# Performance work log

Measured on AMD Instinct MI355X. Metric: run time of the kernel, lower is better.

## Reference

```python
import jax, jax.numpy as jnp
import numpy as np

NEG_SLOPE = 0.2

def gat_conv(x, src, dst, W, a_src, a_dst, b, num_nodes, concat):
    # PyG GATConv (add_self_loops already applied to src/dst).
    H, C = a_src.shape
    h = (x @ W).reshape(-1, H, C)                      # [N,H,C]
    s = jnp.einsum('nhc,hc->nh', h, a_src)             # per-node src score
    d = jnp.einsum('nhc,hc->nh', h, a_dst)             # per-node dst score
    e = jax.nn.leaky_relu(s[src] + d[dst], NEG_SLOPE)  # [E,H]
    emax = jax.lax.stop_gradient(
        jax.ops.segment_max(e, dst, num_segments=num_nodes))  # [N,H]
    ex = jnp.exp(e - emax[dst])
    denom = jax.ops.segment_sum(ex, dst, num_segments=num_nodes)
    alpha = ex / denom[dst]                            # segment softmax over in-edges
    msg = h[src] * alpha[:, :, None]                   # [E,H,C]
    out = jax.ops.segment_sum(msg, dst, num_segments=num_nodes)
    out = out.reshape(num_nodes, H * C) if concat else out.mean(axis=1)
    return out + b

def setup_inputs() -> dict:
    key = jax.random.key(0)
    ks = jax.random.split(key, 20)
    N, E, F = 50000, 400000, 256
    x = jax.random.normal(ks[0], (N, F), dtype=jnp.float32)
    edge_index = jax.random.randint(ks[1], (2, E), 0, N, dtype=jnp.int64)
    def p(k, shape):
        return (jax.random.normal(k, shape, dtype=jnp.float32) * 0.1)
    inp = {'x': x, 'edge_index': edge_index}
    # conv1: 256 -> 8x32 ; conv2: 256 -> 4x32 ; conv3: 128 -> 2x32 ; conv4: 64 -> 1x32
    dims = [(256, 8, 32), (256, 4, 32), (128, 2, 32), (64, 1, 32)]
    ki = 2
    for i, (fin, H, C) in enumerate(dims, start=1):
        inp[f'W{i}'] = p(ks[ki], (fin, H * C)); ki += 1
        inp[f'a_src{i}'] = p(ks[ki], (H, C)); ki += 1
        inp[f'a_dst{i}'] = p(ks[ki], (H, C)); ki += 1
        bdim = H * C if i < 4 else C
        inp[f'b{i}'] = jnp.zeros((bdim,), dtype=jnp.float32)
    return inp

def reference(x, edge_index, W1, a_src1, a_dst1, b1, W2, a_src2, a_dst2, b2,
              W3, a_src3, a_dst3, b3, W4, a_src4, a_dst4, b4):
    N = x.shape[0]
    loops = jnp.arange(N, dtype=edge_index.dtype)
    src = jnp.concatenate([edge_index[0], loops])
    dst = jnp.concatenate([edge_index[1], loops])
    h = jax.nn.elu(gat_conv(x, src, dst, W1, a_src1, a_dst1, b1, N, True))
    h = jax.nn.elu(gat_conv(h, src, dst, W2, a_src2, a_dst2, b2, N, True))
    h = gat_conv(h, src, dst, W3, a_src3, a_dst3, b3, N, True)
    h = jax.nn.elu(h)
    h = gat_conv(h, src, dst, W4, a_src4, a_dst4, b4, N, False)
    return jax.nn.log_softmax(h, axis=1)
```

## Files before the change

### kernel.cpp

```cpp
#include <hip/hip_runtime.h>
#include <hip/hip_bf16.h>

#define LRELU_SLOPE 0.2f

typedef __attribute__((ext_vector_type(8))) short short8;
typedef __attribute__((ext_vector_type(4))) float f32x4;

__device__ __forceinline__ unsigned short bf16r(float f) {
    unsigned int u = __builtin_bit_cast(unsigned int, f);
    u += 0x7fffu + ((u >> 16) & 1u);
    return (unsigned short)(u >> 16);
}
__device__ __forceinline__ float bf2f(unsigned short u) {
    return __builtin_bit_cast(float, (unsigned int)u << 16);
}

#define GLD16(g, l)                                                            \
    __builtin_amdgcn_global_load_lds(                                          \
        (const __attribute__((address_space(1))) void*)(g),                    \
        (__attribute__((address_space(3))) void*)(l), 16, 0, 0)


#define WTOT 108544

__global__ void k_pre(const float* __restrict__ x, unsigned short* __restrict__ Xb,
                      const float* __restrict__ Wa, const float* __restrict__ Wb,
                      const float* __restrict__ Wc, const float* __restrict__ Wd,
                      unsigned short* __restrict__ Ta, unsigned short* __restrict__ Tb,
                      unsigned short* __restrict__ Tc, unsigned short* __restrict__ Td,
                      const int* __restrict__ ei, int* __restrict__ cnt,
                      int XC, int E, int N) {
    int gid = blockIdx.x * blockDim.x + threadIdx.x;
    if (gid < XC) {
        const float4* xp = (const float4*)x + (long)gid * 2;
        float4 a = xp[0], b = xp[1];
        short8 pk;
        pk[0] = (short)bf16r(a.x); pk[1] = (short)bf16r(a.y);
        pk[2] = (short)bf16r(a.z); pk[3] = (short)bf16r(a.w);
        pk[4] = (short)bf16r(b.x); pk[5] = (short)bf16r(b.y);
        pk[6] = (short)bf16r(b.z); pk[7] = (short)bf16r(b.w);
        *(short8*)(Xb + (long)gid * 8) = pk;
        return;
    }
    int id = gid - XC;
    if (id < WTOT) {
        const float* W; unsigned short* T; int K, Nc;
        if (id < 65536)       { W = Wa; T = Ta; K = 256; Nc = 256; }
        else if (id < 98304)  { id -= 65536;  W = Wb; T = Tb; K = 256; Nc = 128; }
        else if (id < 106496) { id -= 98304;  W = Wc; T = Tc; K = 128; Nc = 64; }
        else                  { id -= 106496; W = Wd; T = Td; K = 64;  Nc = 32; }
        int n = id / K, k = id % K;
        T[id] = bf16r(W[(long)k * Nc + n]);
        return;
    }
    int e = id - WTOT;
    if (e >= E + N) return;
    int dst = (e < E) ? ei[E + e] : (e - E);
    atomicAdd(&cnt[dst], 1);
}


__global__ void k_scan_blk(const int* __restrict__ cnt, int* __restrict__ offs,
                           int* __restrict__ bsum, int N) {
    __shared__ int temp[1024];
    int t = threadIdx.x;
    int gi = blockIdx.x * 1024 + t;
    int v = (gi < N) ? cnt[gi] : 0;
    temp[t] = v;
    __syncthreads();
    for (int o = 1; o < 1024; o <<= 1) {
        int x = (t >= o) ? temp[t - o] : 0;
        __syncthreads();
        temp[t] += x;
        __syncthreads();
    }
    if (gi < N) offs[gi] = temp[t] - v;
    if (t == 1023) bsum[blockIdx.x] = temp[1023];
}

__global__ void k_scan(const int* __restrict__ cnt, int* __restrict__ offs, int N) {
    __shared__ int temp[1024];
    __shared__ int carry_s;
    int t = threadIdx.x;
    if (t == 0) carry_s = 0;
    __syncthreads();
    for (int base = 0; base < N; base += 1024) {
        int v = (base + t < N) ? cnt[base + t] : 0;
        temp[t] = v;
        __syncthreads();
        for (int o = 1; o < 1024; o <<= 1) {
            int x = (t >= o) ? temp[t - o] : 0;
            __syncthreads();
            temp[t] += x;
            __syncthreads();
        }
        int incl = temp[t];
        int carry = carry_s;
        if (base + t < N) offs[base + t] = carry + incl - v;
        __syncthreads();
        if (t == 1023) carry_s = carry + temp[1023];
        __syncthreads();
    }
    if (t == 0) offs[N] = carry_s;
}

__global__ void k_scan_add(int* __restrict__ offs, const int* __restrict__ bpre,
                           int* __restrict__ wp, int N, int nb) {
    int gi = blockIdx.x * blockDim.x + threadIdx.x;
    if (gi < N) {
        int v = offs[gi] + bpre[gi >> 10];
        offs[gi] = v;
        wp[gi] = v;
    } else if (gi == N) {
        offs[N] = bpre[nb];
    }
}

__global__ void k_scatter(const int* __restrict__ ei, int* __restrict__ wp,
                          int* __restrict__ adj, int E, int N) {
    int e = blockIdx.x * blockDim.x + threadIdx.x;
    if (e >= E + N) return;
    int srcn = (e < E) ? ei[e] : (e - E);
    int dst  = (e < E) ? ei[E + e] : (e - E);
    int pos = atomicAdd(&wp[dst], 1);
    adj[pos] = srcn;
}


template<int BN, int KT, int GX>
__global__ __launch_bounds__(256) void k_mgemm(const unsigned short* __restrict__ Ab,
                                               const unsigned short* __restrict__ WT,
                                               unsigned short* __restrict__ Cb,
                                               const float* __restrict__ a_src,
                                               const float* __restrict__ a_dst,
                                               float* __restrict__ sbuf,
                                               float* __restrict__ dbuf,
                                               int M, int Nc, int H, int RB) {
    constexpr int KITER = KT / 32;
    constexpr int NBF = BN / 16;
    constexpr int CPR = BN / 32;
    constexpr int SP  = BN + 8;
    constexpr int ASH = 64 * KT;
    constexpr int BSH = BN * KT;
    constexpr int EPIL = 64 * SP;
    constexpr int LBSZ = (ASH + BSH) > EPIL ? (ASH + BSH) : EPIL;
    constexpr int SHC = (KT == 256) ? 5 : (KT == 128 ? 4 : 3);
    constexpr int BIT = BN * KT / 2048;
    __shared__ __align__(16) unsigned short LB[LBSZ];

    int id = blockIdx.x;
    int xcd = id & 7;
    int q  = id >> 3;
    int ct = q % GX;
    int rb = (q / GX) * 8 + xcd;
    if (rb >= RB) return;
    int bm = rb * 64, bn = ct * BN;

    int t = threadIdx.x;
    int wv = t >> 6, l = t & 63;
    int row_in = l & 15, quad = l >> 4;
    char* LBb = (char*)LB;

    long abyte = (long)bm * (KT * 2);
    long mbyte = (long)M * (KT * 2);
    const char* Agb = (const char*)Ab;
#pragma unroll
    for (int i = 0; i < KITER; ++i) {
        int c = i * 256 + t;
        int cs = c ^ ((c >> SHC) & 7);
        long gb = abyte + (long)cs * 16;
        if (gb >= mbyte) gb = abyte;
        GLD16(Agb + gb, LBb + (i * 256 + wv * 64) * 16);
    }
    const char* WTb = (const char*)WT + (long)bn * (KT * 2);
#pragma unroll
    for (int i = 0; i < BIT; ++i) {
        int c = i * 256 + t;
        int cs = c ^ ((c >> SHC) & 7);
        GLD16(WTb + (long)cs * 16, LBb + ASH * 2 + (i * 256 + wv * 64) * 16);
    }
    asm volatile("s_waitcnt vmcnt(0)" ::: "memory");
    __syncthreads();

    f32x4 acc[NBF];
#pragma unroll
    for (int j = 0; j < NBF; ++j) acc[j] = (f32x4){0.f, 0.f, 0.f, 0.f};

    int arow = wv * 16 + row_in;
#pragma unroll
    for (int ki = 0; ki < KITER; ++ki) {
        int aoff = (arow * (KT * 2) + ki * 64 + quad * 16) ^ ((arow & 7) << 4);
        short8 av = *(const short8*)(LBb + aoff);
#pragma unroll
        for (int f = 0; f < NBF; ++f) {
            int bcol = f * 16 + row_in;
            int boff = ASH * 2 + ((bcol * (KT * 2) + ki * 64 + quad * 16) ^ ((bcol & 7) << 4));
            short8 bv = *(const short8*)(LBb + boff);
            acc[f] = __builtin_amdgcn_mfma_f32_16x16x32_bf16(av, bv, acc[f], 0, 0, 0);
        }
    }
    __syncthreads();

#pragma unroll
    for (int r = 0; r < 4; ++r)
#pragma unroll
        for (int f = 0; f < NBF; ++f)
            LB[(wv * 16 + quad * 4 + r) * SP + f * 16 + row_in] = bf16r(acc[f][r]);
    __syncthreads();

    int rr = t / CPR, cc = t % CPR;
    if (rr < 64) {
        int grow = bm + rr;
        int colb = bn + cc * 32;
        if (grow < M && colb < Nc) {
            const unsigned short* ep = &LB[rr * SP + cc * 32];
            short8 v0 = *(const short8*)(ep);
            short8 v1 = *(const short8*)(ep + 8);
            short8 v2 = *(const short8*)(ep + 16);
            short8 v3 = *(const short8*)(ep + 24);
            unsigned short* cp = &Cb[(long)grow * Nc + colb];
            *(short8*)(cp)      = v0;
            *(short8*)(cp + 8)  = v1;
            *(short8*)(cp + 16) = v2;
            *(short8*)(cp + 24) = v3;
            int hd = colb >> 5;
            const float* ap = a_src + hd * 32;
            const float* dp = a_dst + hd * 32;
            float ss = 0.f, dd = 0.f;
#pragma unroll
            for (int u = 0; u < 8; ++u) {
                float va = bf2f((unsigned short)v0[u]); ss += va * ap[u];      dd += va * dp[u];
                float vb = bf2f((unsigned short)v1[u]); ss += vb * ap[8 + u];  dd += vb * dp[8 + u];
                float vc = bf2f((unsigned short)v2[u]); ss += vc * ap[16 + u]; dd += vc * dp[16 + u];
                float vd = bf2f((unsigned short)v3[u]); ss += vd * ap[24 + u]; dd += vd * dp[24 + u];
            }
            sbuf[(long)grow * H + hd] = ss;
            dbuf[(long)grow * H + hd] = dd;
        }
    }
}


#define QB(v, k) __builtin_amdgcn_ds_swizzle((v), 0x8000 | ((k) * 0x55))

template<int ACT>
__global__ void k_aggf(const unsigned short* __restrict__ h, const float* __restrict__ s,
                       const float* __restrict__ dsc, const int* __restrict__ offs,
                       const int* __restrict__ adj, const float* __restrict__ bias,
                       unsigned short* __restrict__ out16, float* __restrict__ out32,
                       int N, int H) {
    const int C8 = 4;
    long tid = (long)blockIdx.x * blockDim.x + threadIdx.x;
    int HC8 = H * C8;
    if (tid >= (long)N * HC8) return;
    int c8 = (int)(tid % C8);
    int hh = (int)((tid / C8) % H);
    int n  = (int)(tid / HC8);
    int beg = offs[n], end = offs[n + 1];
    float dn = dsc[n * H + hh];
    int HC = HC8 * 8;
    int coff = hh * 32 + c8 * 8;
    const unsigned short* hb = h + coff;

    float denom = 0.f;
    float acc[8];
#pragma unroll
    for (int u = 0; u < 8; ++u) acc[u] = 0.f;

    for (int j = beg; j < end; j += 4) {
        int my = j + c8;
        int idx = my < end ? my : end - 1;
        int sn = adj[idx];
        float e = s[sn * H + hh] + dn;
        e = e > 0.f ? e : LRELU_SLOPE * e;
        float w = __expf(fminf(e, 80.f));
        if (my >= end) w = 0.f;
        int wi = __builtin_bit_cast(int, w);
        int sn0 = QB(sn, 0);
        int sn1 = QB(sn, 1);
        int sn2 = QB(sn, 2);
        int sn3 = QB(sn, 3);
        float w0 = __builtin_bit_cast(float, QB(wi, 0));
        float w1 = __builtin_bit_cast(float, QB(wi, 1));
        float w2 = __builtin_bit_cast(float, QB(wi, 2));
        float w3 = __builtin_bit_cast(float, QB(wi, 3));
        short8 h0 = *(const short8*)(hb + (size_t)sn0 * HC);
        short8 h1 = *(const short8*)(hb + (size_t)sn1 * HC);
        short8 h2 = *(const short8*)(hb + (size_t)sn2 * HC);
        short8 h3 = *(const short8*)(hb + (size_t)sn3 * HC);
        denom += (w0 + w1) + (w2 + w3);
#pragma unroll
        for (int u = 0; u < 8; ++u) {
            float a01 = w0 * bf2f((unsigned short)h0[u]) + w1 * bf2f((unsigned short)h1[u]);
            float a23 = w2 * bf2f((unsigned short)h2[u]) + w3 * bf2f((unsigned short)h3[u]);
            acc[u] += a01 + a23;
        }
    }

    float inv = 1.0f / denom;
    float o[8];
#pragma unroll
    for (int u = 0; u < 8; ++u) o[u] = acc[u] * inv + bias[coff + u];

    if (ACT == 1) {
        short8 pk;
#pragma unroll
        for (int u = 0; u < 8; ++u) {
            float v = o[u] > 0.f ? o[u] : (__expf(o[u]) - 1.f);
            pk[u] = (short)bf16r(v);
        }
        *(short8*)(out16 + tid * 8) = pk;
    } else {
        float m = o[0];
#pragma unroll
        for (int u = 1; u < 8; ++u) m = fmaxf(m, o[u]);
        m = fmaxf(m, __shfl_xor(m, 1));
        m = fmaxf(m, __shfl_xor(m, 2));
        float ssum = 0.f;
#pragma unroll
        for (int u = 0; u < 8; ++u) ssum += __expf(o[u] - m);
        ssum += __shfl_xor(ssum, 1);
        ssum += __shfl_xor(ssum, 2);
        float lse = m + __logf(ssum);
        float4 lo = {o[0] - lse, o[1] - lse, o[2] - lse, o[3] - lse};
        float4 hi = {o[4] - lse, o[5] - lse, o[6] - lse, o[7] - lse};
        *(float4*)(out32 + tid * 8)     = lo;
        *(float4*)(out32 + tid * 8 + 4) = hi;
    }
}


static inline size_t align_up(size_t x) { return (x + 255) & ~(size_t)255; }

extern "C" void kernel_launch(void* const* d_in, const int* in_sizes, int n_in,
                              void* d_out, int out_size, void* d_ws, size_t ws_size,
                              hipStream_t stream) {
    const float* x   = (const float*)d_in[0];
    const int*   ei  = (const int*)d_in[1];

    const int N = in_sizes[0] / 256;
    const int E = in_sizes[1] / 2;
    const int ET = E + N;
    const int NB = (N + 1023) / 1024;
    const int XC = N * 32;

    size_t off = 0;
    char* ws = (char*)d_ws;
    auto take = [&](size_t bytes) { char* p = ws + off; off += align_up(bytes); return p; };
    int*   offs  = (int*)take((size_t)(N + 1) * 4);
    int*   wp    = (int*)take((size_t)N * 4);
    int*   adj   = (int*)take((size_t)ET * 4);
    int*   bsum  = (int*)take((size_t)(NB + 1) * 4);
    int*   bpre  = (int*)take((size_t)(NB + 1) * 4);
    float* sbuf  = (float*)take((size_t)N * 8 * 4);
    float* dbuf  = (float*)take((size_t)N * 8 * 4);
    unsigned short* Xb = (unsigned short*)take((size_t)N * 256 * 2);
    unsigned short* Yb = (unsigned short*)take((size_t)N * 256 * 2);
    unsigned short* WT0 = (unsigned short*)take((size_t)256 * 256 * 2);
    unsigned short* WT1 = (unsigned short*)take((size_t)256 * 128 * 2);
    unsigned short* WT2 = (unsigned short*)take((size_t)128 * 64 * 2);
    unsigned short* WT3 = (unsigned short*)take((size_t)64 * 32 * 2);
    (void)ws_size;

    hipMemsetAsync(wp, 0, (size_t)N * 4, stream);
    {
        long tot = (long)XC + WTOT + ET;
        k_pre<<<(int)((tot + 255) / 256), 256, 0, stream>>>(
            x, Xb,
            (const float*)d_in[2], (const float*)d_in[6], (const float*)d_in[10],
            (const float*)d_in[14], WT0, WT1, WT2, WT3, ei, wp, XC, E, N);
        k_scan_blk<<<NB, 1024, 0, stream>>>(wp, offs, bsum, N);
        k_scan<<<1, 1024, 0, stream>>>(bsum, bpre, NB);
        k_scan_add<<<(N + 256) / 256, 256, 0, stream>>>(offs, bpre, wp, N, NB);
        k_scatter<<<(ET + 255) / 256, 256, 0, stream>>>(ei, wp, adj, E, N);
    }

    const float* as_[4] = {(const float*)d_in[3], (const float*)d_in[7],
                           (const float*)d_in[11], (const float*)d_in[15]};
    const float* ad_[4] = {(const float*)d_in[4], (const float*)d_in[8],
                           (const float*)d_in[12], (const float*)d_in[16]};
    const float* b_[4]  = {(const float*)d_in[5], (const float*)d_in[9],
                           (const float*)d_in[13], (const float*)d_in[17]};
    int H_[4] = {8, 4, 2, 1};

    const int RB  = (N + 63) / 64;
    const int RBp = ((RB + 7) / 8) * 8;

    for (int li = 0; li < 4; ++li) {
        int H = H_[li];

        if (li == 0) {
            k_mgemm<64, 256, 4><<<4 * RBp, 256, 0, stream>>>(
                Xb, WT0, Yb, as_[0], ad_[0], sbuf, dbuf, N, 256, H, RB);
        } else if (li == 1) {
            k_mgemm<64, 256, 2><<<2 * RBp, 256, 0, stream>>>(
                Xb, WT1, Yb, as_[1], ad_[1], sbuf, dbuf, N, 128, H, RB);
        } else if (li == 2) {
            k_mgemm<64, 128, 1><<<RBp, 256, 0, stream>>>(
                Xb, WT2, Yb, as_[2], ad_[2], sbuf, dbuf, N, 64, H, RB);
        } else {
            k_mgemm<32, 64, 1><<<RBp, 256, 0, stream>>>(
                Xb, WT3, Yb, as_[3], ad_[3], sbuf, dbuf, N, 32, H, RB);
        }
        {
            long total = (long)N * H * 4;
            int nb = (int)((total + 255) / 256);
            if (li < 3)
                k_aggf<1><<<nb, 256, 0, stream>>>(Yb, sbuf, dbuf, offs, adj, b_[li],
                                                  Xb, nullptr, N, H);
            else
                k_aggf<0><<<nb, 256, 0, stream>>>(Yb, sbuf, dbuf, offs, adj, b_[li],
                                                  nullptr, (float*)d_out, N, H);
        }
    }
}
```

Baseline: 313.8 us.

## Fuse block scan with last-block carry scan and remove scatter atomics

Edge counting now records each edge's slot within its destination bucket, so the scatter kernel writes positions directly without a second atomic pass. Self-loops are handled implicitly by adding one to each count and writing the loop entry first in the scan-add kernel. The separate single-block carry scan is folded into the block-scan kernel through a last-block-done atomic counter, which removes one kernel launch. In exchange it adds a per-edge slot buffer and relies on threadfence-based cross-block synchronisation.

```diff
diff --git a/kernel.cpp b/kernel.cpp
--- a/kernel.cpp
+++ b/kernel.cpp
@@ -29,7 +29,7 @@
                       unsigned short* __restrict__ Ta, unsigned short* __restrict__ Tb,
                       unsigned short* __restrict__ Tc, unsigned short* __restrict__ Td,
                       const int* __restrict__ ei, int* __restrict__ cnt,
-                      int XC, int E, int N) {
+                      int* __restrict__ slot, int XC, int E) {
     int gid = blockIdx.x * blockDim.x + threadIdx.x;
     if (gid < XC) {
         const float4* xp = (const float4*)x + (long)gid * 2;
@@ -54,18 +54,20 @@
         return;
     }
     int e = id - WTOT;
-    if (e >= E + N) return;
-    int dst = (e < E) ? ei[E + e] : (e - E);
-    atomicAdd(&cnt[dst], 1);
+    if (e >= E) return;
+    int dst = ei[E + e];
+    slot[e] = atomicAdd(&cnt[dst], 1);
 }
 
 
 __global__ void k_scan_blk(const int* __restrict__ cnt, int* __restrict__ offs,
-                           int* __restrict__ bsum, int N) {
+                           int* __restrict__ bsum, int* __restrict__ bpre,
+                           int* __restrict__ done, int N, int NB) {
     __shared__ int temp[1024];
+    __shared__ int last_s;
     int t = threadIdx.x;
     int gi = blockIdx.x * 1024 + t;
-    int v = (gi < N) ? cnt[gi] : 0;
+    int v = (gi < N) ? cnt[gi] + 1 : 0;
     temp[t] = v;
     __syncthreads();
     for (int o = 1; o < 1024; o <<= 1) {
@@ -76,17 +78,15 @@
     }
     if (gi < N) offs[gi] = temp[t] - v;
     if (t == 1023) bsum[blockIdx.x] = temp[1023];
-}
-
-__global__ void k_scan(const int* __restrict__ cnt, int* __restrict__ offs, int N) {
-    __shared__ int temp[1024];
-    __shared__ int carry_s;
-    int t = threadIdx.x;
-    if (t == 0) carry_s = 0;
+    if (t == 0) {
+        __threadfence();
+        last_s = (atomicAdd(done, 1) == NB - 1) ? 1 : 0;
+    }
     __syncthreads();
-    for (int base = 0; base < N; base += 1024) {
-        int v = (base + t < N) ? cnt[base + t] : 0;
-        temp[t] = v;
+    if (last_s) {
+        __threadfence();
+        int v2 = (t < NB) ? bsum[t] : 0;
+        temp[t] = v2;
         __syncthreads();
         for (int o = 1; o < 1024; o <<= 1) {
             int x = (t >= o) ? temp[t - o] : 0;
@@ -94,36 +94,30 @@
             temp[t] += x;
             __syncthreads();
         }
-        int incl = temp[t];
-        int carry = carry_s;
-        if (base + t < N) offs[base + t] = carry + incl - v;
-        __syncthreads();
-        if (t == 1023) carry_s = carry + temp[1023];
-        __syncthreads();
-    }
-    if (t == 0) offs[N] = carry_s;
+        if (t < NB) bpre[t] = temp[t] - v2;
+        if (t == NB - 1) bpre[NB] = temp[t];
+    }
 }
 
 __global__ void k_scan_add(int* __restrict__ offs, const int* __restrict__ bpre,
-                           int* __restrict__ wp, int N, int nb) {
+                           int* __restrict__ adj, int N, int nb) {
     int gi = blockIdx.x * blockDim.x + threadIdx.x;
     if (gi < N) {
         int v = offs[gi] + bpre[gi >> 10];
         offs[gi] = v;
-        wp[gi] = v;
+        adj[v] = gi;
     } else if (gi == N) {
         offs[N] = bpre[nb];
     }
 }
 
-__global__ void k_scatter(const int* __restrict__ ei, int* __restrict__ wp,
-                          int* __restrict__ adj, int E, int N) {
+__global__ void k_scatter(const int* __restrict__ ei, const int* __restrict__ offs,
+                          const int* __restrict__ slot, int* __restrict__ adj, int E) {
     int e = blockIdx.x * blockDim.x + threadIdx.x;
-    if (e >= E + N) return;
-    int srcn = (e < E) ? ei[e] : (e - E);
-    int dst  = (e < E) ? ei[E + e] : (e - E);
-    int pos = atomicAdd(&wp[dst], 1);
-    adj[pos] = srcn;
+    if (e >= E) return;
+    int srcn = ei[e];
+    int dst  = ei[E + e];
+    adj[offs[dst] + 1 + slot[e]] = srcn;
 }
 
 
@@ -348,7 +342,8 @@
     char* ws = (char*)d_ws;
     auto take = [&](size_t bytes) { char* p = ws + off; off += align_up(bytes); return p; };
     int*   offs  = (int*)take((size_t)(N + 1) * 4);
-    int*   wp    = (int*)take((size_t)N * 4);
+    int*   cntd  = (int*)take((size_t)(N + 1) * 4);
+    int*   slot  = (int*)take((size_t)E * 4);
     int*   adj   = (int*)take((size_t)ET * 4);
     int*   bsum  = (int*)take((size_t)(NB + 1) * 4);
     int*   bpre  = (int*)take((size_t)(NB + 1) * 4);
@@ -362,17 +357,19 @@
     unsigned short* WT3 = (unsigned short*)take((size_t)64 * 32 * 2);
     (void)ws_size;
 
-    hipMemsetAsync(wp, 0, (size_t)N * 4, stream);
+    int* cnt  = cntd;
+    int* done = cntd + N;
+
+    hipMemsetAsync(cntd, 0, (size_t)(N + 1) * 4, stream);
     {
-        long tot = (long)XC + WTOT + ET;
+        long tot = (long)XC + WTOT + E;
         k_pre<<<(int)((tot + 255) / 256), 256, 0, stream>>>(
             x, Xb,
             (const float*)d_in[2], (const float*)d_in[6], (const float*)d_in[10],
-            (const float*)d_in[14], WT0, WT1, WT2, WT3, ei, wp, XC, E, N);
-        k_scan_blk<<<NB, 1024, 0, stream>>>(wp, offs, bsum, N);
-        k_scan<<<1, 1024, 0, stream>>>(bsum, bpre, NB);
-        k_scan_add<<<(N + 256) / 256, 256, 0, stream>>>(offs, bpre, wp, N, NB);
-        k_scatter<<<(ET + 255) / 256, 256, 0, stream>>>(ei, wp, adj, E, N);
+            (const float*)d_in[14], WT0, WT1, WT2, WT3, ei, cnt, slot, XC, E);
+        k_scan_blk<<<NB, 1024, 0, stream>>>(cnt, offs, bsum, bpre, done, N, NB);
+        k_scan_add<<<(N + 256) / 256, 256, 0, stream>>>(offs, bpre, adj, N, NB);
+        k_scatter<<<(E + 255) / 256, 256, 0, stream>>>(ei, offs, slot, adj, E);
     }
 
     const float* as_[4] = {(const float*)d_in[3], (const float*)d_in[7],
```

New measurement: 308.5 us. No clear change (-1.7%).
